# Kernel tuning notes

Measured on AMD Instinct MI355X. Metric: run time of the kernel, lower is better.

The kernel has to match this reference:

```python
import jax, jax.numpy as jnp
import numpy as np

N = 65536          # number of atoms (routing tokens)
NUM_SPECIES = 4    # number of per-species expert models
D_IN, D_HID, D_OUT = 256, 1024, 256


def setup_inputs() -> dict:
    key = jax.random.key(0)
    k = jax.random.split(key, 6)
    x = jax.random.normal(k[0], (N, D_IN), dtype=jnp.float32)
    central_species = jax.random.randint(k[1], (N,), 0, NUM_SPECIES, dtype=jnp.int64)
    # Per-species 2-layer MLP experts, stacked along species axis.
    W1 = jax.random.normal(k[2], (NUM_SPECIES, D_IN, D_HID), dtype=jnp.float32) * (1.0 / np.sqrt(D_IN))
    b1 = jnp.zeros((NUM_SPECIES, D_HID), dtype=jnp.float32)
    W2 = jax.random.normal(k[3], (NUM_SPECIES, D_HID, D_OUT), dtype=jnp.float32) * (1.0 / np.sqrt(D_HID))
    b2 = jnp.zeros((NUM_SPECIES, D_OUT), dtype=jnp.float32)
    return {"x": x, "central_species": central_species, "W1": W1, "b1": b1, "W2": W2, "b2": b2}


def reference(x, central_species, W1, b1, W2, b2):
    # Equivalent to: split rows by species (CentralSplitter), apply the
    # species-specific submodel, scatter results back by mask (CentralUniter).
    # Dense-compute-and-select expression: every row receives exactly the
    # output of its own species' expert, identical math to masked gather/scatter.
    num_species = W1.shape[0]
    out = jnp.zeros((x.shape[0], W2.shape[-1]), dtype=x.dtype)
    for s in range(num_species):  # small fixed expert count
        h = jax.nn.silu(x @ W1[s] + b1[s])          # [N, D_HID]
        y = h @ W2[s] + b2[s]                       # [N, D_OUT]
        sel = (central_species == s)[:, None]
        out = out + jnp.where(sel, y, jnp.zeros_like(y))
    return out
```

## Files before the change

kernel.cpp:

```cpp
#include <hip/hip_runtime.h>
#include <hip/hip_bf16.h>


#define N_ATOMS 65536
#define D_IN 256
#define D_HID 1024
#define D_OUT 256
#define TPS 1024

typedef __attribute__((ext_vector_type(8))) short short8;
typedef __attribute__((ext_vector_type(4))) float float4e;

#define WS_BUCKET_OFF 256
#define WS_W1_OFF 1048832
#define WS_W2_OFF 3145984

__device__ __forceinline__ short f2bf(float f) {
  unsigned u = __builtin_bit_cast(unsigned, f);
  unsigned r = (u + 0x7FFFu + ((u >> 16) & 1u)) >> 16;
  return (short)r;
}

__global__ void prep_kernel(const float* __restrict__ W1, const float* __restrict__ W2,
                            short* __restrict__ w1sw, short* __restrict__ w2sw,
                            int* __restrict__ cnt) {
  int gid = blockIdx.x * 256 + threadIdx.x;
  if (gid < 64) cnt[gid] = 0;
  int lane = gid & 63;
  int lr = lane & 15;
  int lk = (lane >> 4) * 8;
  if (gid < 131072) {
    int ks = (gid >> 6) & 7;
    int nt = (gid >> 9) & 63;
    int s  = gid >> 15;
    const float* src = W1 + ((size_t)(s * 256 + ks * 32 + lk)) * 1024 + nt * 16 + lr;
    short8 v;
    for (int j = 0; j < 8; ++j) v[j] = f2bf(src[(size_t)j * 1024]);
    *(short8*)(w1sw + (size_t)gid * 8) = v;
  } else {
    int g = gid - 131072;
    int kt = (g >> 6) & 31;
    int nt = (g >> 11) & 15;
    int s  = g >> 15;
    const float* src = W2 + ((size_t)(s * 1024 + kt * 32 + lk)) * 256 + nt * 16 + lr;
    short8 v;
    for (int j = 0; j < 8; ++j) v[j] = f2bf(src[(size_t)j * 256]);
    *(short8*)(w2sw + (size_t)g * 8) = v;
  }
}

__global__ void count_fill_kernel(const int* __restrict__ species,
                                  int* __restrict__ cnt, int* __restrict__ bucket) {
  int tid = threadIdx.x;
  int i = blockIdx.x * 256 + tid;
  int s = species[i] & 3;
  int lane = tid & 63, wid = tid >> 6;
  __shared__ int wcnt[4][4];
  __shared__ int wbase[4][4];
  unsigned long long m0 = __ballot(s == 0);
  unsigned long long m1 = __ballot(s == 1);
  unsigned long long m2 = __ballot(s == 2);
  unsigned long long m3 = __ballot(s == 3);
  if (lane == 0) {
    wcnt[wid][0] = __popcll(m0); wcnt[wid][1] = __popcll(m1);
    wcnt[wid][2] = __popcll(m2); wcnt[wid][3] = __popcll(m3);
  }
  __syncthreads();
  if (tid < 4) {
    int ss = tid;
    int c0 = wcnt[0][ss], c1 = wcnt[1][ss], c2 = wcnt[2][ss], c3 = wcnt[3][ss];
    int base = atomicAdd(&cnt[ss * 16], c0 + c1 + c2 + c3);
    wbase[0][ss] = base;
    wbase[1][ss] = base + c0;
    wbase[2][ss] = base + c0 + c1;
    wbase[3][ss] = base + c0 + c1 + c2;
  }
  __syncthreads();
  unsigned long long below = (1ull << lane) - 1ull;
  int rank = 0;
  if (s == 0) rank = __popcll(m0 & below);
  if (s == 1) rank = __popcll(m1 & below);
  if (s == 2) rank = __popcll(m2 & below);
  if (s == 3) rank = __popcll(m3 & below);
  bucket[s * N_ATOMS + wbase[wid][s] + rank] = i;
}

#define XS_STRIDE 280
#define HS_STRIDE 152
__global__ __launch_bounds__(256, 2) void fused_kernel(
    const float* __restrict__ x, const int* __restrict__ cntArr,
    const int* __restrict__ bucket, const short* __restrict__ w1sw,
    const short* __restrict__ w2sw, const float* __restrict__ b1,
    const float* __restrict__ b2, float* __restrict__ out) {
  int s = blockIdx.x >> 10;
  int t = blockIdx.x & (TPS - 1);
  int cnt = cntArr[s * 16];
  int r0 = t * 64;
  if (r0 >= cnt) return;
  int nrows = min(64, cnt - r0);
  const int* buck = bucket + s * N_ATOMS + r0;

  __shared__ short Xs[64 * XS_STRIDE];
  __shared__ short Hs[2][64 * HS_STRIDE];

  int tid = threadIdx.x;

  for (int i = 0; i < 8; ++i) {
    int id = tid + i * 256;
    int r = id >> 5;
    int g = id & 31;
    short8 v = {};
    if (r < nrows) {
      const float4* src = (const float4*)(x + (size_t)buck[r] * D_IN + g * 8);
      float4 f0 = src[0];
      float4 f1 = src[1];
      v[0] = f2bf(f0.x); v[1] = f2bf(f0.y); v[2] = f2bf(f0.z); v[3] = f2bf(f0.w);
      v[4] = f2bf(f1.x); v[5] = f2bf(f1.y); v[6] = f2bf(f1.z); v[7] = f2bf(f1.w);
    }
    *(short8*)(Xs + r * XS_STRIDE + g * 8) = v;
  }

  int lane = tid & 63;
  int wid = tid >> 6;
  int lr = lane & 15;
  int lk = (lane >> 4) * 8;
  int lq = (lane >> 4) * 4;

  float bias1[8][2];
  #pragma unroll
  for (int c = 0; c < 8; ++c)
    #pragma unroll
    for (int ct = 0; ct < 2; ++ct)
      bias1[c][ct] = b1[s * D_HID + c * 128 + wid * 32 + ct * 16 + lr];
  float bias2[4];
  #pragma unroll
  for (int ct = 0; ct < 4; ++ct)
    bias2[ct] = b2[s * D_OUT + wid * 64 + ct * 16 + lr];

  short8 b1f[16];
  #pragma unroll
  for (int ks = 0; ks < 8; ++ks)
    #pragma unroll
    for (int ct = 0; ct < 2; ++ct) {
      int nt = 0 * 8 + wid * 2 + ct;
      b1f[ks * 2 + ct] = *(const short8*)(w1sw + ((size_t)((s * 64 + nt) * 8 + ks)) * 512 + lane * 8);
    }

  __syncthreads();

  float4e accY[4][4] = {};

  for (int c = 0; c < 8; ++c) {
    float4e acc1[4][2] = {};
    #pragma unroll
    for (int ks = 0; ks < 8; ++ks) {
      short8 a[4];
      #pragma unroll
      for (int rt = 0; rt < 4; ++rt)
        a[rt] = *(const short8*)(Xs + (rt * 16 + lr) * XS_STRIDE + ks * 32 + lk);
      #pragma unroll
      for (int rt = 0; rt < 4; ++rt)
        #pragma unroll
        for (int ct = 0; ct < 2; ++ct)
          acc1[rt][ct] = __builtin_amdgcn_mfma_f32_16x16x32_bf16(a[rt], b1f[ks * 2 + ct], acc1[rt][ct], 0, 0, 0);
    }
    short8 b2f[16];
    #pragma unroll
    for (int ks = 0; ks < 4; ++ks)
      #pragma unroll
      for (int ct = 0; ct < 4; ++ct) {
        int nt = wid * 4 + ct;
        int kt = c * 4 + ks;
        b2f[ks * 4 + ct] = *(const short8*)(w2sw + ((size_t)((s * 16 + nt) * 32 + kt)) * 512 + lane * 8);
      }
    short* hsb = Hs[c & 1];
    #pragma unroll
    for (int ct = 0; ct < 2; ++ct) {
      int nloc = wid * 32 + ct * 16 + lr;
      float bias = bias1[c][ct];
      #pragma unroll
      for (int rt = 0; rt < 4; ++rt) {
        float4e v4 = acc1[rt][ct];
        #pragma unroll
        for (int q = 0; q < 4; ++q) {
          float pre = v4[q] + bias;
          float val = pre / (1.0f + __expf(-pre));
          hsb[(rt * 16 + lq + q) * HS_STRIDE + nloc] = f2bf(val);
        }
      }
    }
    __syncthreads();
    if (c < 7) {
      #pragma unroll
      for (int ks = 0; ks < 8; ++ks)
        #pragma unroll
        for (int ct = 0; ct < 2; ++ct) {
          int nt = (c + 1) * 8 + wid * 2 + ct;
          b1f[ks * 2 + ct] = *(const short8*)(w1sw + ((size_t)((s * 64 + nt) * 8 + ks)) * 512 + lane * 8);
        }
    }
    #pragma unroll
    for (int ks = 0; ks < 4; ++ks) {
      short8 a[4];
      #pragma unroll
      for (int rt = 0; rt < 4; ++rt)
        a[rt] = *(const short8*)(hsb + (rt * 16 + lr) * HS_STRIDE + ks * 32 + lk);
      #pragma unroll
      for (int rt = 0; rt < 4; ++rt)
        #pragma unroll
        for (int ct = 0; ct < 4; ++ct)
          accY[rt][ct] = __builtin_amdgcn_mfma_f32_16x16x32_bf16(a[rt], b2f[ks * 4 + ct], accY[rt][ct], 0, 0, 0);
    }
  }

  #pragma unroll
  for (int ct = 0; ct < 4; ++ct) {
    int n = wid * 64 + ct * 16 + lr;
    float bias = bias2[ct];
    #pragma unroll
    for (int rt = 0; rt < 4; ++rt) {
      #pragma unroll
      for (int q = 0; q < 4; ++q) {
        int r = rt * 16 + lq + q;
        if (r < nrows)
          out[(size_t)buck[r] * D_OUT + n] = accY[rt][ct][q] + bias;
      }
    }
  }
}

extern "C" void kernel_launch(void* const* d_in, const int* in_sizes, int n_in,
                              void* d_out, int out_size, void* d_ws, size_t ws_size,
                              hipStream_t stream) {
  const float* x  = (const float*)d_in[0];
  const int* spc  = (const int*)d_in[1];
  const float* W1 = (const float*)d_in[2];
  const float* b1 = (const float*)d_in[3];
  const float* W2 = (const float*)d_in[4];
  const float* b2 = (const float*)d_in[5];
  float* out = (float*)d_out;

  int*   cnt    = (int*)d_ws;
  int*   bucket = (int*)((char*)d_ws + WS_BUCKET_OFF);
  short* w1sw   = (short*)((char*)d_ws + WS_W1_OFF);
  short* w2sw   = (short*)((char*)d_ws + WS_W2_OFF);

  prep_kernel<<<1024, 256, 0, stream>>>(W1, W2, w1sw, w2sw, cnt);
  count_fill_kernel<<<N_ATOMS / 256, 256, 0, stream>>>(spc, cnt, bucket);
  fused_kernel<<<4 * TPS, 256, 0, stream>>>(x, cnt, bucket, w1sw, w2sw, b1, b2, out);
}
```

Measured before the change: 255.8 us.

## Widen hidden chunks to 256, drop register prefetch, vectorize weight prep

The fused MLP kernel now processes the hidden dimension in 4 chunks of 256 columns instead of 8 of 128. The hidden tile becomes a single larger LDS buffer, and weight fragments are loaded per k-step instead of being prefetched across chunks in registers. This halves the number of barriers and phases and raises the MFMA work per A-fragment load, but it loses the overlap from W1 prefetching and adds a barrier before each H write. The prep kernel switches to float4 coalesced reads of the weights with strided 2-byte scattered writes, and runs on half as many threads.

```diff
diff --git a/kernel.cpp b/kernel.cpp
--- a/kernel.cpp
+++ b/kernel.cpp
@@ -26,27 +26,36 @@
                             int* __restrict__ cnt) {
   int gid = blockIdx.x * 256 + threadIdx.x;
   if (gid < 64) cnt[gid] = 0;
-  int lane = gid & 63;
-  int lr = lane & 15;
-  int lk = (lane >> 4) * 8;
-  if (gid < 131072) {
-    int ks = (gid >> 6) & 7;
-    int nt = (gid >> 9) & 63;
-    int s  = gid >> 15;
-    const float* src = W1 + ((size_t)(s * 256 + ks * 32 + lk)) * 1024 + nt * 16 + lr;
-    short8 v;
-    for (int j = 0; j < 8; ++j) v[j] = f2bf(src[(size_t)j * 1024]);
-    *(short8*)(w1sw + (size_t)gid * 8) = v;
+  float vals[16];
+  short* dst;
+  if (gid < 65536) {
+    int nt = gid & 63;
+    int k  = (gid >> 6) & 255;
+    int s  = gid >> 14;
+    const float4* src = (const float4*)(W1 + ((size_t)(s * 256 + k)) * 1024 + nt * 16);
+    float4 v0 = src[0], v1 = src[1], v2 = src[2], v3 = src[3];
+    vals[0]=v0.x; vals[1]=v0.y; vals[2]=v0.z; vals[3]=v0.w;
+    vals[4]=v1.x; vals[5]=v1.y; vals[6]=v1.z; vals[7]=v1.w;
+    vals[8]=v2.x; vals[9]=v2.y; vals[10]=v2.z; vals[11]=v2.w;
+    vals[12]=v3.x; vals[13]=v3.y; vals[14]=v3.z; vals[15]=v3.w;
+    int ks = k >> 5, kk = k & 31, g = kk >> 3, j = kk & 7;
+    dst = w1sw + ((size_t)((s * 64 + nt) * 8 + ks)) * 512 + g * 128 + j;
   } else {
-    int g = gid - 131072;
-    int kt = (g >> 6) & 31;
-    int nt = (g >> 11) & 15;
-    int s  = g >> 15;
-    const float* src = W2 + ((size_t)(s * 1024 + kt * 32 + lk)) * 256 + nt * 16 + lr;
-    short8 v;
-    for (int j = 0; j < 8; ++j) v[j] = f2bf(src[(size_t)j * 256]);
-    *(short8*)(w2sw + (size_t)g * 8) = v;
-  }
+    int g2 = gid - 65536;
+    int nt = g2 & 15;
+    int k  = (g2 >> 4) & 1023;
+    int s  = g2 >> 14;
+    const float4* src = (const float4*)(W2 + ((size_t)(s * 1024 + k)) * 256 + nt * 16);
+    float4 v0 = src[0], v1 = src[1], v2 = src[2], v3 = src[3];
+    vals[0]=v0.x; vals[1]=v0.y; vals[2]=v0.z; vals[3]=v0.w;
+    vals[4]=v1.x; vals[5]=v1.y; vals[6]=v1.z; vals[7]=v1.w;
+    vals[8]=v2.x; vals[9]=v2.y; vals[10]=v2.z; vals[11]=v2.w;
+    vals[12]=v3.x; vals[13]=v3.y; vals[14]=v3.z; vals[15]=v3.w;
+    int kt = k >> 5, kk = k & 31, g = kk >> 3, j = kk & 7;
+    dst = w2sw + ((size_t)((s * 16 + nt) * 32 + kt)) * 512 + g * 128 + j;
+  }
+  #pragma unroll
+  for (int lr = 0; lr < 16; ++lr) dst[lr * 8] = f2bf(vals[lr]);
 }
 
 __global__ void count_fill_kernel(const int* __restrict__ species,
@@ -86,7 +95,7 @@
 }
 
 #define XS_STRIDE 280
-#define HS_STRIDE 152
+#define HS_STRIDE 264
 __global__ __launch_bounds__(256, 2) void fused_kernel(
     const float* __restrict__ x, const int* __restrict__ cntArr,
     const int* __restrict__ bucket, const short* __restrict__ w1sw,
@@ -101,7 +110,7 @@
   const int* buck = bucket + s * N_ATOMS + r0;
 
   __shared__ short Xs[64 * XS_STRIDE];
-  __shared__ short Hs[2][64 * HS_STRIDE];
+  __shared__ short Hs[64 * HS_STRIDE];
 
   int tid = threadIdx.x;
 
@@ -126,34 +135,32 @@
   int lk = (lane >> 4) * 8;
   int lq = (lane >> 4) * 4;
 
-  float bias1[8][2];
-  #pragma unroll
-  for (int c = 0; c < 8; ++c)
-    #pragma unroll
-    for (int ct = 0; ct < 2; ++ct)
-      bias1[c][ct] = b1[s * D_HID + c * 128 + wid * 32 + ct * 16 + lr];
+  float bias1[4][4];
+  #pragma unroll
+  for (int c = 0; c < 4; ++c)
+    #pragma unroll
+    for (int ct = 0; ct < 4; ++ct)
+      bias1[c][ct] = b1[s * D_HID + c * 256 + wid * 64 + ct * 16 + lr];
   float bias2[4];
   #pragma unroll
   for (int ct = 0; ct < 4; ++ct)
     bias2[ct] = b2[s * D_OUT + wid * 64 + ct * 16 + lr];
 
-  short8 b1f[16];
-  #pragma unroll
-  for (int ks = 0; ks < 8; ++ks)
-    #pragma unroll
-    for (int ct = 0; ct < 2; ++ct) {
-      int nt = 0 * 8 + wid * 2 + ct;
-      b1f[ks * 2 + ct] = *(const short8*)(w1sw + ((size_t)((s * 64 + nt) * 8 + ks)) * 512 + lane * 8);
-    }
-
   __syncthreads();
 
   float4e accY[4][4] = {};
 
-  for (int c = 0; c < 8; ++c) {
-    float4e acc1[4][2] = {};
+  #pragma unroll
+  for (int c = 0; c < 4; ++c) {
+    float4e acc1[4][4] = {};
     #pragma unroll
     for (int ks = 0; ks < 8; ++ks) {
+      short8 b[4];
+      #pragma unroll
+      for (int ct = 0; ct < 4; ++ct) {
+        int nt = c * 16 + wid * 4 + ct;
+        b[ct] = *(const short8*)(w1sw + ((size_t)((s * 64 + nt) * 8 + ks)) * 512 + lane * 8);
+      }
       short8 a[4];
       #pragma unroll
       for (int rt = 0; rt < 4; ++rt)
@@ -161,22 +168,13 @@
       #pragma unroll
       for (int rt = 0; rt < 4; ++rt)
         #pragma unroll
-        for (int ct = 0; ct < 2; ++ct)
-          acc1[rt][ct] = __builtin_amdgcn_mfma_f32_16x16x32_bf16(a[rt], b1f[ks * 2 + ct], acc1[rt][ct], 0, 0, 0);
-    }
-    short8 b2f[16];
-    #pragma unroll
-    for (int ks = 0; ks < 4; ++ks)
-      #pragma unroll
-      for (int ct = 0; ct < 4; ++ct) {
-        int nt = wid * 4 + ct;
-        int kt = c * 4 + ks;
-        b2f[ks * 4 + ct] = *(const short8*)(w2sw + ((size_t)((s * 16 + nt) * 32 + kt)) * 512 + lane * 8);
-      }
-    short* hsb = Hs[c & 1];
-    #pragma unroll
-    for (int ct = 0; ct < 2; ++ct) {
-      int nloc = wid * 32 + ct * 16 + lr;
+        for (int ct = 0; ct < 4; ++ct)
+          acc1[rt][ct] = __builtin_amdgcn_mfma_f32_16x16x32_bf16(a[rt], b[ct], acc1[rt][ct], 0, 0, 0);
+    }
+    __syncthreads();
+    #pragma unroll
+    for (int ct = 0; ct < 4; ++ct) {
+      int nloc = wid * 64 + ct * 16 + lr;
       float bias = bias1[c][ct];
       #pragma unroll
       for (int rt = 0; rt < 4; ++rt) {
@@ -185,31 +183,29 @@
         for (int q = 0; q < 4; ++q) {
           float pre = v4[q] + bias;
           float val = pre / (1.0f + __expf(-pre));
-          hsb[(rt * 16 + lq + q) * HS_STRIDE + nloc] = f2bf(val);
+          Hs[(rt * 16 + lq + q) * HS_STRIDE + nloc] = f2bf(val);
         }
       }
     }
     __syncthreads();
-    if (c < 7) {
-      #pragma unroll
-      for (int ks = 0; ks < 8; ++ks)
-        #pragma unroll
-        for (int ct = 0; ct < 2; ++ct) {
-          int nt = (c + 1) * 8 + wid * 2 + ct;
-          b1f[ks * 2 + ct] = *(const short8*)(w1sw + ((size_t)((s * 64 + nt) * 8 + ks)) * 512 + lane * 8);
-        }
-    }
-    #pragma unroll
-    for (int ks = 0; ks < 4; ++ks) {
+    #pragma unroll
+    for (int ks = 0; ks < 8; ++ks) {
+      short8 b[4];
+      #pragma unroll
+      for (int ct = 0; ct < 4; ++ct) {
+        int nt = wid * 4 + ct;
+        int kt = c * 8 + ks;
+        b[ct] = *(const short8*)(w2sw + ((size_t)((s * 16 + nt) * 32 + kt)) * 512 + lane * 8);
+      }
       short8 a[4];
       #pragma unroll
       for (int rt = 0; rt < 4; ++rt)
-        a[rt] = *(const short8*)(hsb + (rt * 16 + lr) * HS_STRIDE + ks * 32 + lk);
+        a[rt] = *(const short8*)(Hs + (rt * 16 + lr) * HS_STRIDE + ks * 32 + lk);
       #pragma unroll
       for (int rt = 0; rt < 4; ++rt)
         #pragma unroll
         for (int ct = 0; ct < 4; ++ct)
-          accY[rt][ct] = __builtin_amdgcn_mfma_f32_16x16x32_bf16(a[rt], b2f[ks * 4 + ct], accY[rt][ct], 0, 0, 0);
+          accY[rt][ct] = __builtin_amdgcn_mfma_f32_16x16x32_bf16(a[rt], b[ct], accY[rt][ct], 0, 0, 0);
     }
   }
 
@@ -245,7 +241,7 @@
   short* w1sw   = (short*)((char*)d_ws + WS_W1_OFF);
   short* w2sw   = (short*)((char*)d_ws + WS_W2_OFF);
 
-  prep_kernel<<<1024, 256, 0, stream>>>(W1, W2, w1sw, w2sw, cnt);
+  prep_kernel<<<512, 256, 0, stream>>>(W1, W2, w1sw, w2sw, cnt);
   count_fill_kernel<<<N_ATOMS / 256, 256, 0, stream>>>(spc, cnt, bucket);
   fused_kernel<<<4 * TPS, 256, 0, stream>>>(x, cnt, bucket, w1sw, w2sw, b1, b2, out);
 }
```

After: 284.8 us. 1.11x slower.
